# Optimization experiments

Measured on AMD Instinct MI355X. Metric: run time of the kernel, lower is better.

## Reference

```python
import jax, jax.numpy as jnp
import numpy as np

N = 4096; B = 4; NPB = N // B; K = 16
C = 128; COUT = 128; LMAX = 2; L = (LMAX + 1) ** 2  # 9 SH coefficients
H = 8; A = 8; V = 16; HV = H * V
F = 256; NB = 128; FD = 256; CUTOFF = 3.0
E = N * K

def _silu(x):
    return x * jax.nn.sigmoid(x)

def _mish(x):
    return x * jnp.tanh(jax.nn.softplus(x))

def _rms_norm(x, gamma):
    # degree-wise RMS over channel dim, x: [N, L, C]
    s = jnp.sqrt(jnp.mean(x * x, axis=-1, keepdims=True) + 1e-6)
    return x / s * gamma

def _rot_l1(x, R):
    # rotate the l=1 block (coeffs 1:4) of x [E, L, C] by R [E, 3, 3]
    l1 = jnp.einsum('eij,ejc->eic', R, x[:, 1:4, :])
    return jnp.concatenate([x[:, :1, :], l1, x[:, 4:, :]], axis=1)

def _knn(coord, batch):
    d2 = jnp.sum((coord[:, None, :] - coord[None, :, :]) ** 2, axis=-1)  # [N,N]
    same = batch[:, None] == batch[None, :]
    big = jnp.asarray(1e9, d2.dtype)
    d2 = jnp.where(same, d2, big)
    d2 = d2.at[jnp.arange(N), jnp.arange(N)].set(big)
    neg, idx = jax.lax.top_k(-d2, K)
    dist = jnp.sqrt(jnp.maximum(-neg, 0.0))
    edge_src = idx.reshape(-1)                       # [E]
    edge_dst = jnp.repeat(jnp.arange(N), K)          # [E]
    valid = (dist <= CUTOFF).reshape(-1)
    return edge_src, edge_dst, valid

def _edge_rot_mat(edge_vec):
    # deterministic rotation aligning each edge with the y-axis (eSCN-style)
    nx = edge_vec / (jnp.linalg.norm(edge_vec, axis=-1, keepdims=True) + 1e-12)
    ref = jnp.where(jnp.abs(nx[:, :1]) < 0.9,
                    jnp.array([1.0, 0.0, 0.0], nx.dtype),
                    jnp.array([0.0, 1.0, 0.0], nx.dtype))
    nz = jnp.cross(nx, ref)
    nz = nz / (jnp.linalg.norm(nz, axis=-1, keepdims=True) + 1e-12)
    ny = jnp.cross(nz, nx)
    return jnp.stack([nz, nx, ny], axis=1)  # [E,3,3]; R @ edge_dir = e_y

def _forward(node_coord, node_emb, batch, condition,
             W_e1, b_e1, W_e2, b_e2, W_src, W_dst, w_a, W_v, W_o,
             gamma1, gamma2, W_g, W_f1, W_f2, W_film, b_film):
    # dynamic KNN graph; geometry detached as in original (edge_vec.detach())
    coord_g = jax.lax.stop_gradient(node_coord)
    edge_src, edge_dst, valid = _knn(coord_g, batch)
    edge_vec = coord_g[edge_src] - coord_g[edge_dst]                  # [E,3]
    edge_len = jnp.linalg.norm(edge_vec, axis=-1)                     # [E]
    R = _edge_rot_mat(edge_vec)                                       # [E,3,3]
    # gaussian radial basis -> per-edge embedding
    mu = jnp.linspace(0.0, CUTOFF, NB)
    sigma = CUTOFF / NB
    rbf = jnp.exp(-0.5 * ((edge_len[:, None] - mu) / sigma) ** 2)     # [E,NB]
    edge_h = _silu(rbf @ W_e1 + b_e1) @ W_e2 + b_e2                   # [E,HV]
    # equivariant attention (rotate into edge frame, attend, rotate back)
    x_src = _rot_l1(node_emb[edge_src], R)                            # [E,L,C]
    q = node_emb[edge_dst, 0] @ W_dst + x_src[:, 0] @ W_src           # [E,H*A]
    logits = jnp.einsum('eha,ha->eh', _silu(q).reshape(E, H, A), w_a)
    logits = jnp.where(valid[:, None], logits, -1e9)
    m = jax.ops.segment_max(logits, edge_dst, num_segments=N)
    ex = jnp.exp(logits - m[edge_dst])
    den = jax.ops.segment_sum(ex, edge_dst, num_segments=N)
    attn = ex / (den[edge_dst] + 1e-9)                                # [E,H]
    v = jnp.einsum('elc,cv->elv', x_src, W_v) * edge_h[:, None, :]    # [E,L,HV]
    v = v.reshape(E, L, H, V) * attn[:, None, :, None]
    msg = _rot_l1(v.reshape(E, L, HV), jnp.swapaxes(R, 1, 2))         # back to global frame
    agg = jax.ops.segment_sum(msg, edge_dst, num_segments=N)          # [N,L,HV]
    x = node_emb + jnp.einsum('nlv,vc->nlc', agg, W_o)
    # FFN with separable S2 (scalar-gated) activation
    h = _rms_norm(x, gamma2)
    gate = _silu(h[:, 0] @ W_g)                                       # [N,F]
    hid = jnp.einsum('nlc,cf->nlf', h, W_f1) * gate[:, None, :]
    x = x + jnp.einsum('nlf,fo->nlo', hid, W_f2)
    x = _rms_norm(x, gamma1)
    # FiLM conditioning over flattened (L*C) per batch element
    film = _mish(condition) @ W_film + b_film                         # [B, 2*L*COUT]
    w, bfi = film[:, :L * COUT], film[:, L * COUT:]
    c = x.reshape(B, NPB, L * COUT) * w[:, None, :] + bfi[:, None, :]
    return c.reshape(N, L, COUT)

def setup_inputs():
    key = jax.random.key(0)
    ks = jax.random.split(key, 16)
    node_coord = jax.random.uniform(ks[0], (N, 3)) * 2.0
    node_emb = jax.random.normal(ks[1], (N, L, C)) * 0.1
    batch = jnp.arange(N, dtype=jnp.int64 if jax.config.jax_enable_x64 else jnp.int32) // NPB
    condition = jax.random.normal(ks[2], (B, FD))
    s = lambda d: 1.0 / np.sqrt(d)
    return {
        'node_coord': node_coord, 'node_emb': node_emb, 'batch': batch, 'condition': condition,
        'W_e1': jax.random.normal(ks[3], (NB, 128)) * s(NB), 'b_e1': jnp.zeros((128,)),
        'W_e2': jax.random.normal(ks[4], (128, HV)) * s(128), 'b_e2': jnp.zeros((HV,)),
        'W_src': jax.random.normal(ks[5], (C, H * A)) * s(C),
        'W_dst': jax.random.normal(ks[6], (C, H * A)) * s(C),
        'w_a': jax.random.normal(ks[7], (H, A)) * s(A),
        'W_v': jax.random.normal(ks[8], (C, HV)) * s(C),
        'W_o': jax.random.normal(ks[9], (HV, C)) * s(HV),
        'gamma1': jnp.ones((C,)), 'gamma2': jnp.ones((C,)),
        'W_g': jax.random.normal(ks[10], (C, F)) * s(C),
        'W_f1': jax.random.normal(ks[11], (C, F)) * s(C),
        'W_f2': jax.random.normal(ks[12], (F, COUT)) * s(F),
        'W_film': jax.random.normal(ks[13], (FD, 2 * L * COUT)) * s(FD),
        'b_film': jnp.zeros((2 * L * COUT,)),
    }

def reference(node_coord, node_emb, batch, condition,
              W_e1, b_e1, W_e2, b_e2, W_src, W_dst, w_a, W_v, W_o,
              gamma1, gamma2, W_g, W_f1, W_f2, W_film, b_film):
    out = _forward(node_coord, node_emb, batch, condition,
                   W_e1, b_e1, W_e2, b_e2, W_src, W_dst, w_a, W_v, W_o,
                   gamma1, gamma2, W_g, W_f1, W_f2, W_film, b_film)
    return (node_coord, out, batch)
```

## Files before the change

### kernel.cpp

```cpp
#include <hip/hip_runtime.h>

#define NNODE 4096
#define NPB   1024

__device__ __forceinline__ float siluf(float x){ return x / (1.0f + expf(-x)); }

__global__ __launch_bounds__(256) void k_film(const float* __restrict__ cond,
                                              const float* __restrict__ Wfilm,
                                              const float* __restrict__ bfilm,
                                              float* __restrict__ filmG){
  __shared__ float mL[256];
  int b = blockIdx.y;
  int t = threadIdx.x;
  int j = blockIdx.x*256 + t;
  float x = cond[b*256 + t];
  float sp = fmaxf(x, 0.f) + log1pf(expf(-fabsf(x)));
  mL[t] = x * tanhf(sp);
  __syncthreads();
  if(j >= 2304) return;
  float acc = bfilm[j];
  for(int i=0;i<256;i++) acc += mL[i] * Wfilm[i*2304 + j];
  filmG[b*2304 + j] = acc;
}

__global__ __launch_bounds__(128) void k_pre(const float* __restrict__ emb,
                                             const float* __restrict__ Wv,
                                             const float* __restrict__ Wsrc,
                                             const float* __restrict__ Wdst,
                                             float* __restrict__ ZG,
                                             float* __restrict__ QsG,
                                             float* __restrict__ QdG){
  __shared__ __align__(16) float Es[1152];
  const int n = blockIdx.x;
  const int t = threadIdx.x;
  {
    const float4* src = (const float4*)(emb + (size_t)n*1152);
    float4* dst = (float4*)Es;
    for(int idx=t; idx<288; idx+=128) dst[idx] = src[idx];
  }
  __syncthreads();
  const int l0 = (t>>6)*4;
  const int c0 = (t&63)*2;
  float z[5][2];
  #pragma unroll
  for(int il=0;il<5;il++){ z[il][0]=0.f; z[il][1]=0.f; }
  for(int c4=0;c4<32;c4++){
    float2 wv0 = *(const float2*)&Wv[(c4*4+0)*128 + c0];
    float2 wv1 = *(const float2*)&Wv[(c4*4+1)*128 + c0];
    float2 wv2 = *(const float2*)&Wv[(c4*4+2)*128 + c0];
    float2 wv3 = *(const float2*)&Wv[(c4*4+3)*128 + c0];
    #pragma unroll
    for(int il=0;il<5;il++){
      float4 x4 = *(const float4*)&Es[(l0+il)*128 + c4*4];
      z[il][0] += x4.x*wv0.x + x4.y*wv1.x + x4.z*wv2.x + x4.w*wv3.x;
      z[il][1] += x4.x*wv0.y + x4.y*wv1.y + x4.z*wv2.y + x4.w*wv3.y;
    }
  }
  #pragma unroll
  for(int il=0;il<5;il++){
    float2 o; o.x = z[il][0]; o.y = z[il][1];
    *(float2*)&ZG[(size_t)n*1152 + (l0+il)*128 + c0] = o;
  }
  {
    const float* W = (t < 64) ? Wsrc : Wdst;
    const int col = t & 63;
    float q = 0.f;
    for(int c=0;c<128;c++) q += Es[c] * W[c*64 + col];
    if(t < 64) QsG[n*64 + col] = q;
    else       QdG[n*64 + col] = q;
  }
}

#define E_HD   0
#define E_QS   0
#define E_QD   1024
#define E_LG   1088
#define E_SX   1216
#define E_EH   2048
#define E_RBW  4096
#define E_AT   4352
#define E_KI   4480
#define E_KD   4496
#define E_LEN  4512
#define E_VL   4528
#define E_W0   4544
#define E_NPF  4608
__global__ __launch_bounds__(256) void k_edge(
    const float* __restrict__ coord,
    const float* __restrict__ We1, const float* __restrict__ be1,
    const float* __restrict__ We2, const float* __restrict__ be2,
    const float* __restrict__ wa,
    const float* __restrict__ Qs, const float* __restrict__ Qd,
    const float* __restrict__ Z,
    float* __restrict__ out){
  __shared__ __align__(16) float S[2*E_NPF];
  int* Si = (int*)S;
  const int t = threadIdx.x;
  const int h = t >> 7;
  const int u = t & 127;
  const int n = blockIdx.x*2 + h;
  const int base = n & ~(NPB - 1);
  const int self = n - base;
  const int NP = h * E_NPF;
  float* aggG = out + 12288;

  for(int idx = t; idx < 3072; idx += 256) S[idx] = coord[base*3 + idx];
  __syncthreads();
  const float cx = S[self*3+0];
  const float cy = S[self*3+1];
  const float cz = S[self*3+2];
  if((t & 64) == 0){
    int lane = t & 63;
    float d2a[16]; int ida[16];
    for(int q=0;q<16;q++){
      int j = lane + q*64;
      float dx = __fsub_rn(S[j*3+0], cx);
      float dy = __fsub_rn(S[j*3+1], cy);
      float dz = __fsub_rn(S[j*3+2], cz);
      float d2 = __fadd_rn(__fadd_rn(__fmul_rn(dx,dx), __fmul_rn(dy,dy)), __fmul_rn(dz,dz));
      if(j == self) d2 = 3e38f;
      d2a[q] = d2; ida[q] = j;
    }
    for(int r=0;r<16;r++){
      float bd = d2a[0]; int bi = ida[0];
      for(int q=1;q<16;q++){
        bool bet = (d2a[q] < bd) || (d2a[q] == bd && ida[q] < bi);
        if(bet){ bd = d2a[q]; bi = ida[q]; }
      }
      for(int s=1;s<64;s<<=1){
        float od = __shfl_xor(bd, s, 64);
        int   oi = __shfl_xor(bi, s, 64);
        bool bet = (od < bd) || (od == bd && oi < bi);
        if(bet){ bd = od; bi = oi; }
      }
      if(lane == 0){ Si[NP + E_KI + r] = bi; S[NP + E_KD + r] = bd; }
      for(int q=0;q<16;q++) if(ida[q] == bi) d2a[q] = 3e38f;
    }
  }
  __syncthreads();

  if(u < 16){
    float len = __fsqrt_rn(S[NP + E_KD + u]);
    S[NP + E_LEN + u] = len;
    S[NP + E_VL + u]  = (len <= 3.0f) ? 1.0f : 0.0f;
    int i0 = (int)(len * (127.0f/3.0f) + 0.5f);
    int w0 = i0 - 7;
    w0 = w0 < 0 ? 0 : (w0 > 112 ? 112 : w0);
    Si[NP + E_W0 + u] = w0;
  }
  for(int idx = u; idx < 1024; idx += 128){
    int e = idx >> 6, ha = idx & 63;
    int src = base + Si[NP + E_KI + e];
    S[NP + E_QS + idx] = Qs[src*64 + ha];
  }
  if(u < 64) S[NP + E_QD + u] = Qd[n*64 + u];
  __syncthreads();

  {
    int e = u >> 3, hh = u & 7;
    float s = 0.f;
    #pragma unroll
    for(int a=0;a<8;a++){
      float q = S[NP + E_QD + hh*8 + a] + S[NP + E_QS + e*64 + hh*8 + a];
      s += siluf(q) * wa[hh*8 + a];
    }
    S[NP + E_LG + u] = (S[NP + E_VL + e] > 0.5f) ? s : -1e9f;

    const float step = 3.0f/127.0f;
    const float sigma = 3.0f/128.0f;
    for(int idx = u; idx < 256; idx += 128){
      int e2 = idx >> 4, w = idx & 15;
      int bin = Si[NP + E_W0 + e2] + w;
      float d = (S[NP + E_LEN + e2] - step*(float)bin) / sigma;
      S[NP + E_RBW + idx] = expf(-0.5f*d*d);
    }
  }
  __syncthreads();

  if(u < 8){
    float m = -3e38f;
    for(int r=0;r<16;r++) m = fmaxf(m, S[NP + E_LG + r*8 + u]);
    S[NP + E_SX + u] = m;
  }
  __syncthreads();
  {
    float ex = expf(S[NP + E_LG + u] - S[NP + E_SX + (u & 7)]);
    __syncthreads();
    S[NP + E_LG + u] = ex;
    __syncthreads();
    if(u < 8){
      float d = 0.f;
      for(int r=0;r<16;r++) d += S[NP + E_LG + r*8 + u];
      S[NP + E_SX + 8 + u] = d;
    }
    __syncthreads();
    S[NP + E_AT + u] = ex / (S[NP + E_SX + 8 + (u & 7)] + 1e-9f);
  }
  __syncthreads();

  const int w2 = (t >> 6) & 1;
  const int u2 = t & 63;
  const int c0 = u2*2;
  {
    float a4[8][2]; int b0[8];
    #pragma unroll
    for(int k=0;k<8;k++){ a4[k][0]=0.f; a4[k][1]=0.f; b0[k] = Si[NP + E_W0 + 8*w2 + k]; }
    for(int wi=0; wi<16; wi++){
      #pragma unroll
      for(int k=0;k<8;k++){
        float rb = S[NP + E_RBW + (8*w2+k)*16 + wi];
        float2 we = *(const float2*)&We1[(b0[k] + wi)*128 + c0];
        a4[k][0] = fmaf(rb, we.x, a4[k][0]);
        a4[k][1] = fmaf(rb, we.y, a4[k][1]);
      }
    }
    float2 be = *(const float2*)&be1[c0];
    #pragma unroll
    for(int k=0;k<8;k++){
      float2 o; o.x = siluf(a4[k][0] + be.x); o.y = siluf(a4[k][1] + be.y);
      *(float2*)&S[NP + E_HD + (8*w2+k)*128 + c0] = o;
    }
  }

  {
    float a5[8][2];
    #pragma unroll
    for(int k=0;k<8;k++){ a5[k][0]=0.f; a5[k][1]=0.f; }
    for(int c4=0;c4<32;c4++){
      float2 w0 = *(const float2*)&We2[(c4*4+0)*128 + c0];
      float2 w1 = *(const float2*)&We2[(c4*4+1)*128 + c0];
      float2 w2v= *(const float2*)&We2[(c4*4+2)*128 + c0];
      float2 w3 = *(const float2*)&We2[(c4*4+3)*128 + c0];
      #pragma unroll
      for(int k=0;k<8;k++){
        float4 h4 = *(const float4*)&S[NP + E_HD + (8*w2+k)*128 + c4*4];
        a5[k][0] += h4.x*w0.x + h4.y*w1.x + h4.z*w2v.x + h4.w*w3.x;
        a5[k][1] += h4.x*w0.y + h4.y*w1.y + h4.z*w2v.y + h4.w*w3.y;
      }
    }
    float2 be = *(const float2*)&be2[c0];
    #pragma unroll
    for(int k=0;k<8;k++){
      float2 o; o.x = a5[k][0] + be.x; o.y = a5[k][1] + be.y;
      *(float2*)&S[NP + E_EH + (8*w2+k)*128 + c0] = o;
    }
  }
  __syncthreads();

  {
    float ag[9][2];
    #pragma unroll
    for(int l=0;l<9;l++){ ag[l][0]=0.f; ag[l][1]=0.f; }
    #pragma unroll
    for(int k=0;k<8;k++){
      int e = 8*w2 + k;
      const float* zp = &Z[(size_t)(base + Si[NP + E_KI + e])*1152 + c0];
      float at = S[NP + E_AT + e*8 + (c0>>4)];
      float2 eh2 = *(const float2*)&S[NP + E_EH + e*128 + c0];
      float sc0 = eh2.x * at;
      float sc1 = eh2.y * at;
      #pragma unroll
      for(int l=0;l<9;l++){
        float2 z2 = *(const float2*)&zp[l*128];
        ag[l][0] = fmaf(z2.x, sc0, ag[l][0]);
        ag[l][1] = fmaf(z2.y, sc1, ag[l][1]);
      }
    }
    if(w2 == 0){
      #pragma unroll
      for(int l=0;l<9;l++){
        float2 o; o.x = ag[l][0]; o.y = ag[l][1];
        *(float2*)&S[NP + l*128 + c0] = o;
      }
    }
    __syncthreads();
    if(w2 == 1){
      #pragma unroll
      for(int l=0;l<9;l++){
        float2 p = *(const float2*)&S[NP + l*128 + c0];
        float2 o; o.x = ag[l][0] + p.x; o.y = ag[l][1] + p.y;
        *(float2*)&aggG[(size_t)n*1152 + l*128 + c0] = o;
      }
    }
  }
}

#define FW_ACT 0
#define FW_HID 1152
#define FW_SZ  2304
__global__ __launch_bounds__(256) void k_ffn(
    const float* __restrict__ emb,
    const float* __restrict__ Wo,
    const float* __restrict__ g1, const float* __restrict__ g2,
    const float* __restrict__ Wg, const float* __restrict__ Wf1,
    const float* __restrict__ Wf2,
    const float* __restrict__ filmG,
    float* __restrict__ out){
  __shared__ __align__(16) float S[4*FW_SZ];
  const int t = threadIdx.x;
  const int rg = t >> 6;
  const int u2 = t & 63;
  const int c0 = u2*2;
  const int n = blockIdx.x*4 + rg;
  float* W_ = &S[rg*FW_SZ];
  float* aggG = out + 12288;

  {
    const float4* src = (const float4*)(aggG + (size_t)n*1152);
    float4* dst = (float4*)&W_[FW_ACT];
    for(int i=u2;i<288;i+=64) dst[i] = src[i];
  }

  float x[9][2];
  #pragma unroll
  for(int l=0;l<9;l++){ x[l][0]=0.f; x[l][1]=0.f; }
  for(int c4=0;c4<32;c4++){
    float2 w0 = *(const float2*)&Wo[(c4*4+0)*128 + c0];
    float2 w1 = *(const float2*)&Wo[(c4*4+1)*128 + c0];
    float2 w2 = *(const float2*)&Wo[(c4*4+2)*128 + c0];
    float2 w3 = *(const float2*)&Wo[(c4*4+3)*128 + c0];
    #pragma unroll
    for(int l=0;l<9;l++){
      float4 a4 = *(const float4*)&W_[FW_ACT + l*128 + c4*4];
      x[l][0] += a4.x*w0.x + a4.y*w1.x + a4.z*w2.x + a4.w*w3.x;
      x[l][1] += a4.x*w0.y + a4.y*w1.y + a4.z*w2.y + a4.w*w3.y;
    }
  }

  float g2a = g2[c0], g2b = g2[c0+1];
  #pragma unroll
  for(int l=0;l<9;l++){
    float2 e2 = *(const float2*)&emb[(size_t)n*1152 + l*128 + c0];
    x[l][0] += e2.x; x[l][1] += e2.y;
    float sq = x[l][0]*x[l][0] + x[l][1]*x[l][1];
    #pragma unroll
    for(int s=1;s<64;s<<=1) sq += __shfl_xor(sq, s, 64);
    float ss = sqrtf(sq/128.f + 1e-6f);
    float2 o; o.x = x[l][0]/ss*g2a; o.y = x[l][1]/ss*g2b;
    *(float2*)&W_[FW_ACT + l*128 + c0] = o;
  }

  float ha[2][9][2]; float ga[2][2];
  #pragma unroll
  for(int ft=0;ft<2;ft++){
    ga[ft][0]=0.f; ga[ft][1]=0.f;
    #pragma unroll
    for(int l=0;l<9;l++){ ha[ft][l][0]=0.f; ha[ft][l][1]=0.f; }
  }
  for(int c4=0;c4<32;c4++){
    float2 wf[2][4], wg_[2][4];
    #pragma unroll
    for(int ft=0;ft<2;ft++)
      #pragma unroll
      for(int i=0;i<4;i++){
        wf[ft][i]  = *(const float2*)&Wf1[(c4*4+i)*256 + ft*128 + c0];
        wg_[ft][i] = *(const float2*)&Wg [(c4*4+i)*256 + ft*128 + c0];
      }
    float4 h0 = *(const float4*)&W_[FW_ACT + 0*128 + c4*4];
    #pragma unroll
    for(int ft=0;ft<2;ft++){
      ga[ft][0] += h0.x*wg_[ft][0].x + h0.y*wg_[ft][1].x + h0.z*wg_[ft][2].x + h0.w*wg_[ft][3].x;
      ga[ft][1] += h0.x*wg_[ft][0].y + h0.y*wg_[ft][1].y + h0.z*wg_[ft][2].y + h0.w*wg_[ft][3].y;
      ha[ft][0][0] += h0.x*wf[ft][0].x + h0.y*wf[ft][1].x + h0.z*wf[ft][2].x + h0.w*wf[ft][3].x;
      ha[ft][0][1] += h0.x*wf[ft][0].y + h0.y*wf[ft][1].y + h0.z*wf[ft][2].y + h0.w*wf[ft][3].y;
    }
    #pragma unroll
    for(int l=1;l<9;l++){
      float4 h4 = *(const float4*)&W_[FW_ACT + l*128 + c4*4];
      #pragma unroll
      for(int ft=0;ft<2;ft++){
        ha[ft][l][0] += h4.x*wf[ft][0].x + h4.y*wf[ft][1].x + h4.z*wf[ft][2].x + h4.w*wf[ft][3].x;
        ha[ft][l][1] += h4.x*wf[ft][0].y + h4.y*wf[ft][1].y + h4.z*wf[ft][2].y + h4.w*wf[ft][3].y;
      }
    }
  }

  #pragma unroll
  for(int ft=0;ft<2;ft++){
    float gx = siluf(ga[ft][0]), gy = siluf(ga[ft][1]);
    #pragma unroll
    for(int l=0;l<9;l++){
      float2 o; o.x = ha[ft][l][0]*gx; o.y = ha[ft][l][1]*gy;
      *(float2*)&W_[FW_HID + l*128 + c0] = o;
    }
    for(int f4=0;f4<32;f4++){
      float2 w0 = *(const float2*)&Wf2[(ft*128 + f4*4+0)*128 + c0];
      float2 w1 = *(const float2*)&Wf2[(ft*128 + f4*4+1)*128 + c0];
      float2 w2 = *(const float2*)&Wf2[(ft*128 + f4*4+2)*128 + c0];
      float2 w3 = *(const float2*)&Wf2[(ft*128 + f4*4+3)*128 + c0];
      #pragma unroll
      for(int l=0;l<9;l++){
        float4 h4 = *(const float4*)&W_[FW_HID + l*128 + f4*4];
        x[l][0] += h4.x*w0.x + h4.y*w1.x + h4.z*w2.x + h4.w*w3.x;
        x[l][1] += h4.x*w0.y + h4.y*w1.y + h4.z*w2.y + h4.w*w3.y;
      }
    }
  }

  {
    float g1a = g1[c0], g1b = g1[c0+1];
    int b = n >> 10;
    #pragma unroll
    for(int l=0;l<9;l++){
      float sq = x[l][0]*x[l][0] + x[l][1]*x[l][1];
      #pragma unroll
      for(int s=1;s<64;s<<=1) sq += __shfl_xor(sq, s, 64);
      float ss = sqrtf(sq/128.f + 1e-6f);
      float2 fw = *(const float2*)&filmG[b*2304 + l*128 + c0];
      float2 fb = *(const float2*)&filmG[b*2304 + 1152 + l*128 + c0];
      float2 o;
      o.x = x[l][0]/ss*g1a*fw.x + fb.x;
      o.y = x[l][1]/ss*g1b*fw.y + fb.y;
      *(float2*)&out[12288 + (size_t)n*1152 + l*128 + c0] = o;
    }
  }
}

__global__ __launch_bounds__(256) void k_copy(const float* __restrict__ coord,
                                              float* __restrict__ out){
  int i = blockIdx.x*256 + threadIdx.x;
  if(i < 12288) out[i] = coord[i];
  int n = i - 12288;
  if(n >= 0 && n < 4096) out[12288 + 4718592 + n] = (float)(n >> 10);
}

extern "C" void kernel_launch(void* const* d_in, const int* in_sizes, int n_in,
                              void* d_out, int out_size, void* d_ws, size_t ws_size,
                              hipStream_t stream) {
  const float* coord = (const float*)d_in[0];
  const float* emb   = (const float*)d_in[1];
  const float* cond  = (const float*)d_in[3];
  const float* We1   = (const float*)d_in[4];
  const float* be1   = (const float*)d_in[5];
  const float* We2   = (const float*)d_in[6];
  const float* be2   = (const float*)d_in[7];
  const float* Wsrc  = (const float*)d_in[8];
  const float* Wdst  = (const float*)d_in[9];
  const float* wa    = (const float*)d_in[10];
  const float* Wv    = (const float*)d_in[11];
  const float* Wo    = (const float*)d_in[12];
  const float* g1    = (const float*)d_in[13];
  const float* g2    = (const float*)d_in[14];
  const float* Wg    = (const float*)d_in[15];
  const float* Wf1   = (const float*)d_in[16];
  const float* Wf2   = (const float*)d_in[17];
  const float* Wfilm = (const float*)d_in[18];
  const float* bfilm = (const float*)d_in[19];

  float* outf  = (float*)d_out;
  float* filmG = (float*)d_ws;
  float* QsG   = filmG + 9216;
  float* QdG   = QsG + 262144;
  float* ZG    = QdG + 262144;

  k_film<<<dim3(9,4), 256, 0, stream>>>(cond, Wfilm, bfilm, filmG);
  k_pre<<<NNODE, 128, 0, stream>>>(emb, Wv, Wsrc, Wdst, ZG, QsG, QdG);
  k_edge<<<NNODE/2, 256, 0, stream>>>(coord, We1, be1, We2, be2, wa,
                                      QsG, QdG, ZG, outf);
  k_ffn<<<NNODE/4, 256, 0, stream>>>(emb, Wo, g1, g2, Wg, Wf1, Wf2,
                                     filmG, outf);
  k_copy<<<64, 256, 0, stream>>>(coord, outf);
}
```

Before: 442.6 us.

## Restructure edge, pre and FFN kernels to one wavefront per node

Result: faster. 410.6 us (-7.2%).

```diff
diff --git a/kernel.cpp b/kernel.cpp
--- a/kernel.cpp
+++ b/kernel.cpp
@@ -23,69 +23,59 @@
   filmG[b*2304 + j] = acc;
 }
 
-__global__ __launch_bounds__(128) void k_pre(const float* __restrict__ emb,
+__global__ __launch_bounds__(256) void k_pre(const float* __restrict__ emb,
                                              const float* __restrict__ Wv,
                                              const float* __restrict__ Wsrc,
                                              const float* __restrict__ Wdst,
                                              float* __restrict__ ZG,
                                              float* __restrict__ QsG,
                                              float* __restrict__ QdG){
-  __shared__ __align__(16) float Es[1152];
-  const int n = blockIdx.x;
   const int t = threadIdx.x;
-  {
-    const float4* src = (const float4*)(emb + (size_t)n*1152);
-    float4* dst = (float4*)Es;
-    for(int idx=t; idx<288; idx+=128) dst[idx] = src[idx];
-  }
-  __syncthreads();
-  const int l0 = (t>>6)*4;
-  const int c0 = (t&63)*2;
-  float z[5][2];
-  #pragma unroll
-  for(int il=0;il<5;il++){ z[il][0]=0.f; z[il][1]=0.f; }
+  const int rg = __builtin_amdgcn_readfirstlane(t >> 6);
+  const int lane = t & 63;
+  const int c0 = lane*2;
+  const int n = blockIdx.x*4 + rg;
+  const float* en = emb + (size_t)n*1152;
+
+  float z[9][2];
+  #pragma unroll
+  for(int l=0;l<9;l++){ z[l][0]=0.f; z[l][1]=0.f; }
   for(int c4=0;c4<32;c4++){
     float2 wv0 = *(const float2*)&Wv[(c4*4+0)*128 + c0];
     float2 wv1 = *(const float2*)&Wv[(c4*4+1)*128 + c0];
     float2 wv2 = *(const float2*)&Wv[(c4*4+2)*128 + c0];
     float2 wv3 = *(const float2*)&Wv[(c4*4+3)*128 + c0];
     #pragma unroll
-    for(int il=0;il<5;il++){
-      float4 x4 = *(const float4*)&Es[(l0+il)*128 + c4*4];
-      z[il][0] += x4.x*wv0.x + x4.y*wv1.x + x4.z*wv2.x + x4.w*wv3.x;
-      z[il][1] += x4.x*wv0.y + x4.y*wv1.y + x4.z*wv2.y + x4.w*wv3.y;
-    }
-  }
-  #pragma unroll
-  for(int il=0;il<5;il++){
-    float2 o; o.x = z[il][0]; o.y = z[il][1];
-    *(float2*)&ZG[(size_t)n*1152 + (l0+il)*128 + c0] = o;
-  }
-  {
-    const float* W = (t < 64) ? Wsrc : Wdst;
-    const int col = t & 63;
-    float q = 0.f;
-    for(int c=0;c<128;c++) q += Es[c] * W[c*64 + col];
-    if(t < 64) QsG[n*64 + col] = q;
-    else       QdG[n*64 + col] = q;
-  }
-}
-
-#define E_HD   0
-#define E_QS   0
-#define E_QD   1024
-#define E_LG   1088
-#define E_SX   1216
-#define E_EH   2048
-#define E_RBW  4096
-#define E_AT   4352
-#define E_KI   4480
-#define E_KD   4496
-#define E_LEN  4512
-#define E_VL   4528
-#define E_W0   4544
-#define E_NPF  4608
-__global__ __launch_bounds__(256) void k_edge(
+    for(int l=0;l<9;l++){
+      float4 x4 = *(const float4*)&en[l*128 + c4*4];
+      z[l][0] += x4.x*wv0.x + x4.y*wv1.x + x4.z*wv2.x + x4.w*wv3.x;
+      z[l][1] += x4.x*wv0.y + x4.y*wv1.y + x4.z*wv2.y + x4.w*wv3.y;
+    }
+  }
+  #pragma unroll
+  for(int l=0;l<9;l++){
+    float2 o; o.x=z[l][0]; o.y=z[l][1];
+    *(float2*)&ZG[(size_t)n*1152 + l*128 + c0] = o;
+  }
+  float qs = 0.f, qd = 0.f;
+  for(int c=0;c<128;c++){
+    float ec = en[c];
+    qs = fmaf(ec, Wsrc[c*64 + lane], qs);
+    qd = fmaf(ec, Wdst[c*64 + lane], qd);
+  }
+  QsG[n*64 + lane] = qs;
+  QdG[n*64 + lane] = qd;
+}
+
+#define E2_HD   0
+#define E2_RB   2048
+#define E2_AT   2304
+#define E2_KI   2432
+#define E2_LEN  2448
+#define E2_VL   2464
+#define E2_W0   2480
+#define E2_NPF  2560
+__global__ __launch_bounds__(128) void k_edge(
     const float* __restrict__ coord,
     const float* __restrict__ We1, const float* __restrict__ be1,
     const float* __restrict__ We2, const float* __restrict__ be2,
@@ -93,36 +83,38 @@
     const float* __restrict__ Qs, const float* __restrict__ Qd,
     const float* __restrict__ Z,
     float* __restrict__ out){
-  __shared__ __align__(16) float S[2*E_NPF];
+  __shared__ __align__(16) float S[2*E2_NPF];
   int* Si = (int*)S;
   const int t = threadIdx.x;
-  const int h = t >> 7;
-  const int u = t & 127;
-  const int n = blockIdx.x*2 + h;
+  const int w = __builtin_amdgcn_readfirstlane(t >> 6);
+  const int lane = t & 63;
+  const int n = blockIdx.x*2 + w;
   const int base = n & ~(NPB - 1);
   const int self = n - base;
-  const int NP = h * E_NPF;
+  const int NP = w * E2_NPF;
+  const int c0 = lane*2;
+  const int myh = lane >> 3;
   float* aggG = out + 12288;
 
-  for(int idx = t; idx < 3072; idx += 256) S[idx] = coord[base*3 + idx];
-  __syncthreads();
-  const float cx = S[self*3+0];
-  const float cy = S[self*3+1];
-  const float cz = S[self*3+2];
-  if((t & 64) == 0){
-    int lane = t & 63;
+  {
+    const float* cb = coord + (size_t)base*3;
+    const float cx = cb[self*3+0];
+    const float cy = cb[self*3+1];
+    const float cz = cb[self*3+2];
     float d2a[16]; int ida[16];
+    #pragma unroll
     for(int q=0;q<16;q++){
       int j = lane + q*64;
-      float dx = __fsub_rn(S[j*3+0], cx);
-      float dy = __fsub_rn(S[j*3+1], cy);
-      float dz = __fsub_rn(S[j*3+2], cz);
+      float dx = __fsub_rn(cb[j*3+0], cx);
+      float dy = __fsub_rn(cb[j*3+1], cy);
+      float dz = __fsub_rn(cb[j*3+2], cz);
       float d2 = __fadd_rn(__fadd_rn(__fmul_rn(dx,dx), __fmul_rn(dy,dy)), __fmul_rn(dz,dz));
       if(j == self) d2 = 3e38f;
       d2a[q] = d2; ida[q] = j;
     }
     for(int r=0;r<16;r++){
       float bd = d2a[0]; int bi = ida[0];
+      #pragma unroll
       for(int q=1;q<16;q++){
         bool bet = (d2a[q] < bd) || (d2a[q] == bd && ida[q] < bi);
         if(bet){ bd = d2a[q]; bi = ida[q]; }
@@ -133,132 +125,118 @@
         bool bet = (od < bd) || (od == bd && oi < bi);
         if(bet){ bd = od; bi = oi; }
       }
-      if(lane == 0){ Si[NP + E_KI + r] = bi; S[NP + E_KD + r] = bd; }
+      if(lane == 0){
+        Si[NP + E2_KI + r] = bi;
+        float len = __fsqrt_rn(bd);
+        S[NP + E2_LEN + r] = len;
+        S[NP + E2_VL + r]  = (len <= 3.0f) ? 1.0f : 0.0f;
+        int i0 = (int)(len * (127.0f/3.0f) + 0.5f);
+        int w0 = i0 - 7;
+        w0 = w0 < 0 ? 0 : (w0 > 112 ? 112 : w0);
+        Si[NP + E2_W0 + r] = w0;
+      }
+      #pragma unroll
       for(int q=0;q<16;q++) if(ida[q] == bi) d2a[q] = 3e38f;
     }
   }
   __syncthreads();
 
-  if(u < 16){
-    float len = __fsqrt_rn(S[NP + E_KD + u]);
-    S[NP + E_LEN + u] = len;
-    S[NP + E_VL + u]  = (len <= 3.0f) ? 1.0f : 0.0f;
-    int i0 = (int)(len * (127.0f/3.0f) + 0.5f);
-    int w0 = i0 - 7;
-    w0 = w0 < 0 ? 0 : (w0 > 112 ? 112 : w0);
-    Si[NP + E_W0 + u] = w0;
-  }
-  for(int idx = u; idx < 1024; idx += 128){
-    int e = idx >> 6, ha = idx & 63;
-    int src = base + Si[NP + E_KI + e];
-    S[NP + E_QS + idx] = Qs[src*64 + ha];
-  }
-  if(u < 64) S[NP + E_QD + u] = Qd[n*64 + u];
-  __syncthreads();
-
   {
-    int e = u >> 3, hh = u & 7;
-    float s = 0.f;
-    #pragma unroll
-    for(int a=0;a<8;a++){
-      float q = S[NP + E_QD + hh*8 + a] + S[NP + E_QS + e*64 + hh*8 + a];
-      s += siluf(q) * wa[hh*8 + a];
-    }
-    S[NP + E_LG + u] = (S[NP + E_VL + e] > 0.5f) ? s : -1e9f;
+    const int e0 = lane >> 3, hh = lane & 7;
+    float4 qda = *(const float4*)&Qd[(size_t)n*64 + hh*8];
+    float4 qdb = *(const float4*)&Qd[(size_t)n*64 + hh*8 + 4];
+    float4 waa = *(const float4*)&wa[hh*8];
+    float4 wab = *(const float4*)&wa[hh*8 + 4];
+    float lg[2];
+    #pragma unroll
+    for(int s=0;s<2;s++){
+      int e = e0 + s*8;
+      int src = base + Si[NP + E2_KI + e];
+      float4 qa = *(const float4*)&Qs[(size_t)src*64 + hh*8];
+      float4 qb = *(const float4*)&Qs[(size_t)src*64 + hh*8 + 4];
+      float sv = siluf(qda.x+qa.x)*waa.x + siluf(qda.y+qa.y)*waa.y
+               + siluf(qda.z+qa.z)*waa.z + siluf(qda.w+qa.w)*waa.w
+               + siluf(qdb.x+qb.x)*wab.x + siluf(qdb.y+qb.y)*wab.y
+               + siluf(qdb.z+qb.z)*wab.z + siluf(qdb.w+qb.w)*wab.w;
+      lg[s] = (S[NP + E2_VL + e] > 0.5f) ? sv : -1e9f;
+    }
+    float m = fmaxf(lg[0], lg[1]);
+    m = fmaxf(m, __shfl_xor(m, 8, 64));
+    m = fmaxf(m, __shfl_xor(m, 16, 64));
+    m = fmaxf(m, __shfl_xor(m, 32, 64));
+    float ex0 = expf(lg[0] - m), ex1 = expf(lg[1] - m);
+    float den = ex0 + ex1;
+    den += __shfl_xor(den, 8, 64);
+    den += __shfl_xor(den, 16, 64);
+    den += __shfl_xor(den, 32, 64);
+    float inv = 1.0f/(den + 1e-9f);
+    S[NP + E2_AT + lane]      = ex0*inv;
+    S[NP + E2_AT + 64 + lane] = ex1*inv;
 
     const float step = 3.0f/127.0f;
     const float sigma = 3.0f/128.0f;
-    for(int idx = u; idx < 256; idx += 128){
-      int e2 = idx >> 4, w = idx & 15;
-      int bin = Si[NP + E_W0 + e2] + w;
-      float d = (S[NP + E_LEN + e2] - step*(float)bin) / sigma;
-      S[NP + E_RBW + idx] = expf(-0.5f*d*d);
+    #pragma unroll
+    for(int k=0;k<4;k++){
+      int idx = lane + k*64;
+      int e = idx >> 4, wi = idx & 15;
+      float len = S[NP + E2_LEN + e];
+      int bin = Si[NP + E2_W0 + e] + wi;
+      float d = (len - step*(float)bin) / sigma;
+      S[NP + E2_RB + idx] = expf(-0.5f*d*d);
     }
   }
   __syncthreads();
 
-  if(u < 8){
-    float m = -3e38f;
-    for(int r=0;r<16;r++) m = fmaxf(m, S[NP + E_LG + r*8 + u]);
-    S[NP + E_SX + u] = m;
+  {
+    float a4[16][2]; int b0e[16];
+    #pragma unroll
+    for(int e=0;e<16;e++){ a4[e][0]=0.f; a4[e][1]=0.f; b0e[e] = Si[NP + E2_W0 + e]; }
+    for(int wi=0; wi<16; wi++){
+      #pragma unroll
+      for(int e=0;e<16;e++){
+        float rb = S[NP + E2_RB + e*16 + wi];
+        float2 we = *(const float2*)&We1[(size_t)(b0e[e] + wi)*128 + c0];
+        a4[e][0] = fmaf(rb, we.x, a4[e][0]);
+        a4[e][1] = fmaf(rb, we.y, a4[e][1]);
+      }
+    }
+    float2 b1v = *(const float2*)&be1[c0];
+    #pragma unroll
+    for(int e=0;e<16;e++){
+      float2 o; o.x = siluf(a4[e][0] + b1v.x); o.y = siluf(a4[e][1] + b1v.y);
+      *(float2*)&S[NP + E2_HD + e*128 + c0] = o;
+    }
   }
   __syncthreads();
+
+  float a5[16][2];
+  #pragma unroll
+  for(int e=0;e<16;e++){ a5[e][0]=0.f; a5[e][1]=0.f; }
+  for(int c4=0;c4<32;c4++){
+    float2 w0 = *(const float2*)&We2[(c4*4+0)*128 + c0];
+    float2 w1 = *(const float2*)&We2[(c4*4+1)*128 + c0];
+    float2 w2 = *(const float2*)&We2[(c4*4+2)*128 + c0];
+    float2 w3 = *(const float2*)&We2[(c4*4+3)*128 + c0];
+    #pragma unroll
+    for(int e=0;e<16;e++){
+      float4 h4 = *(const float4*)&S[NP + E2_HD + e*128 + c4*4];
+      a5[e][0] += h4.x*w0.x + h4.y*w1.x + h4.z*w2.x + h4.w*w3.x;
+      a5[e][1] += h4.x*w0.y + h4.y*w1.y + h4.z*w2.y + h4.w*w3.y;
+    }
+  }
+
   {
-    float ex = expf(S[NP + E_LG + u] - S[NP + E_SX + (u & 7)]);
-    __syncthreads();
-    S[NP + E_LG + u] = ex;
-    __syncthreads();
-    if(u < 8){
-      float d = 0.f;
-      for(int r=0;r<16;r++) d += S[NP + E_LG + r*8 + u];
-      S[NP + E_SX + 8 + u] = d;
-    }
-    __syncthreads();
-    S[NP + E_AT + u] = ex / (S[NP + E_SX + 8 + (u & 7)] + 1e-9f);
-  }
-  __syncthreads();
-
-  const int w2 = (t >> 6) & 1;
-  const int u2 = t & 63;
-  const int c0 = u2*2;
-  {
-    float a4[8][2]; int b0[8];
-    #pragma unroll
-    for(int k=0;k<8;k++){ a4[k][0]=0.f; a4[k][1]=0.f; b0[k] = Si[NP + E_W0 + 8*w2 + k]; }
-    for(int wi=0; wi<16; wi++){
-      #pragma unroll
-      for(int k=0;k<8;k++){
-        float rb = S[NP + E_RBW + (8*w2+k)*16 + wi];
-        float2 we = *(const float2*)&We1[(b0[k] + wi)*128 + c0];
-        a4[k][0] = fmaf(rb, we.x, a4[k][0]);
-        a4[k][1] = fmaf(rb, we.y, a4[k][1]);
-      }
-    }
-    float2 be = *(const float2*)&be1[c0];
-    #pragma unroll
-    for(int k=0;k<8;k++){
-      float2 o; o.x = siluf(a4[k][0] + be.x); o.y = siluf(a4[k][1] + be.y);
-      *(float2*)&S[NP + E_HD + (8*w2+k)*128 + c0] = o;
-    }
-  }
-
-  {
-    float a5[8][2];
-    #pragma unroll
-    for(int k=0;k<8;k++){ a5[k][0]=0.f; a5[k][1]=0.f; }
-    for(int c4=0;c4<32;c4++){
-      float2 w0 = *(const float2*)&We2[(c4*4+0)*128 + c0];
-      float2 w1 = *(const float2*)&We2[(c4*4+1)*128 + c0];
-      float2 w2v= *(const float2*)&We2[(c4*4+2)*128 + c0];
-      float2 w3 = *(const float2*)&We2[(c4*4+3)*128 + c0];
-      #pragma unroll
-      for(int k=0;k<8;k++){
-        float4 h4 = *(const float4*)&S[NP + E_HD + (8*w2+k)*128 + c4*4];
-        a5[k][0] += h4.x*w0.x + h4.y*w1.x + h4.z*w2v.x + h4.w*w3.x;
-        a5[k][1] += h4.x*w0.y + h4.y*w1.y + h4.z*w2v.y + h4.w*w3.y;
-      }
-    }
-    float2 be = *(const float2*)&be2[c0];
-    #pragma unroll
-    for(int k=0;k<8;k++){
-      float2 o; o.x = a5[k][0] + be.x; o.y = a5[k][1] + be.y;
-      *(float2*)&S[NP + E_EH + (8*w2+k)*128 + c0] = o;
-    }
-  }
-  __syncthreads();
-
-  {
+    float2 b2v = *(const float2*)&be2[c0];
     float ag[9][2];
     #pragma unroll
     for(int l=0;l<9;l++){ ag[l][0]=0.f; ag[l][1]=0.f; }
     #pragma unroll
-    for(int k=0;k<8;k++){
-      int e = 8*w2 + k;
-      const float* zp = &Z[(size_t)(base + Si[NP + E_KI + e])*1152 + c0];
-      float at = S[NP + E_AT + e*8 + (c0>>4)];
-      float2 eh2 = *(const float2*)&S[NP + E_EH + e*128 + c0];
-      float sc0 = eh2.x * at;
-      float sc1 = eh2.y * at;
+    for(int e=0;e<16;e++){
+      int src = base + Si[NP + E2_KI + e];
+      const float* zp = &Z[(size_t)src*1152 + c0];
+      float at = S[NP + E2_AT + e*8 + myh];
+      float sc0 = (a5[e][0] + b2v.x) * at;
+      float sc1 = (a5[e][1] + b2v.y) * at;
       #pragma unroll
       for(int l=0;l<9;l++){
         float2 z2 = *(const float2*)&zp[l*128];
@@ -266,21 +244,10 @@
         ag[l][1] = fmaf(z2.y, sc1, ag[l][1]);
       }
     }
-    if(w2 == 0){
-      #pragma unroll
-      for(int l=0;l<9;l++){
-        float2 o; o.x = ag[l][0]; o.y = ag[l][1];
-        *(float2*)&S[NP + l*128 + c0] = o;
-      }
-    }
-    __syncthreads();
-    if(w2 == 1){
-      #pragma unroll
-      for(int l=0;l<9;l++){
-        float2 p = *(const float2*)&S[NP + l*128 + c0];
-        float2 o; o.x = ag[l][0] + p.x; o.y = ag[l][1] + p.y;
-        *(float2*)&aggG[(size_t)n*1152 + l*128 + c0] = o;
-      }
+    #pragma unroll
+    for(int l=0;l<9;l++){
+      float2 o; o.x = ag[l][0]; o.y = ag[l][1];
+      *(float2*)&aggG[(size_t)n*1152 + l*128 + c0] = o;
     }
   }
 }
@@ -298,18 +265,13 @@
     float* __restrict__ out){
   __shared__ __align__(16) float S[4*FW_SZ];
   const int t = threadIdx.x;
-  const int rg = t >> 6;
+  const int rg = __builtin_amdgcn_readfirstlane(t >> 6);
   const int u2 = t & 63;
   const int c0 = u2*2;
   const int n = blockIdx.x*4 + rg;
   float* W_ = &S[rg*FW_SZ];
   float* aggG = out + 12288;
-
-  {
-    const float4* src = (const float4*)(aggG + (size_t)n*1152);
-    float4* dst = (float4*)&W_[FW_ACT];
-    for(int i=u2;i<288;i+=64) dst[i] = src[i];
-  }
+  const float* agp = aggG + (size_t)n*1152;
 
   float x[9][2];
   #pragma unroll
@@ -321,7 +283,7 @@
     float2 w3 = *(const float2*)&Wo[(c4*4+3)*128 + c0];
     #pragma unroll
     for(int l=0;l<9;l++){
-      float4 a4 = *(const float4*)&W_[FW_ACT + l*128 + c4*4];
+      float4 a4 = *(const float4*)&agp[l*128 + c4*4];
       x[l][0] += a4.x*w0.x + a4.y*w1.x + a4.z*w2.x + a4.w*w3.x;
       x[l][1] += a4.x*w0.y + a4.y*w1.y + a4.z*w2.y + a4.w*w3.y;
     }
@@ -454,8 +416,8 @@
   float* ZG    = QdG + 262144;
 
   k_film<<<dim3(9,4), 256, 0, stream>>>(cond, Wfilm, bfilm, filmG);
-  k_pre<<<NNODE, 128, 0, stream>>>(emb, Wv, Wsrc, Wdst, ZG, QsG, QdG);
-  k_edge<<<NNODE/2, 256, 0, stream>>>(coord, We1, be1, We2, be2, wa,
+  k_pre<<<NNODE/4, 256, 0, stream>>>(emb, Wv, Wsrc, Wdst, ZG, QsG, QdG);
+  k_edge<<<NNODE/2, 128, 0, stream>>>(coord, We1, be1, We2, be2, wa,
                                       QsG, QdG, ZG, outf);
   k_ffn<<<NNODE/4, 256, 0, stream>>>(emb, Wo, g1, g2, Wg, Wf1, Wf2,
                                      filmG, outf);
```
